# Kernel tuning notes

Hardware: AMD Instinct MI355X
Metric: run time of the kernel (lower is better)

The kernel has to match this reference:

```python
import jax, jax.numpy as jnp
import numpy as np

T, B, E, H = 2048, 2, 1024, 16

def setup_inputs() -> dict:
    rng = jax.random.key(0)
    ks = jax.random.split(rng, 7)
    s = 0.02
    return {
        "query": jax.random.normal(ks[0], (T, B, E), jnp.float32),
        "key": jax.random.normal(ks[1], (T, B, E), jnp.float32),
        "value": jax.random.normal(ks[2], (T, B, E), jnp.float32),
        "in_proj_weight": jax.random.normal(ks[3], (3 * E, E), jnp.float32) * s,
        "in_proj_bias": jax.random.normal(ks[4], (3 * E,), jnp.float32) * s,
        "out_proj_weight": jax.random.normal(ks[5], (E, E), jnp.float32) * s,
        "out_proj_bias": jax.random.normal(ks[6], (E,), jnp.float32) * s,
    }

def reference(query, key, value, in_proj_weight, in_proj_bias, out_proj_weight, out_proj_bias):
    tgt_len, bsz, embed_dim = query.shape
    num_heads = H
    head_dim = embed_dim // num_heads
    scaling = head_dim ** -0.5
    wq, wk, wv = jnp.split(in_proj_weight, 3, axis=0)
    bq, bk, bv = jnp.split(in_proj_bias, 3, axis=0)
    # projections: F.linear(x, W, b) = x @ W.T + b
    q = (query @ wq.T + bq) * scaling          # (T, B, E)
    k = key @ wk.T + bk                        # (S, B, E)
    v = value @ wv.T + bv                      # (S, B, E)
    # (len, B, E) -> (B*H, len, head_dim), matching torch view+transpose
    def to_heads(x):
        L = x.shape[0]
        return x.reshape(L, bsz * num_heads, head_dim).transpose(1, 0, 2)
    q, k, v = to_heads(q), to_heads(k), to_heads(v)
    scores = jnp.einsum('bqd,bkd->bqk', q, k)  # (B*H, T, S)
    attn = jax.nn.softmax(scores, axis=-1)
    out = jnp.einsum('bqk,bkd->bqd', attn, v)  # (B*H, T, head_dim)
    out = out.transpose(1, 0, 2).reshape(tgt_len, bsz, embed_dim)
    out = out @ out_proj_weight.T + out_proj_bias
    return out
```

## Files before the change

kernel.cpp:

```cpp
#include <hip/hip_runtime.h>
#include <cstdint>
#include <cstddef>

#define QSCALE 0.18033688011112042f

typedef __attribute__((ext_vector_type(8))) short bf16x8;
typedef __attribute__((ext_vector_type(4))) float f32x4;

#define MFMA(a, b, c) __builtin_amdgcn_mfma_f32_16x16x32_bf16(a, b, c, 0, 0, 0)

#define PIPE_SYNC() do {                                   \
    asm volatile("s_waitcnt vmcnt(0)" ::: "memory");       \
    __builtin_amdgcn_sched_barrier(0);                     \
    __builtin_amdgcn_s_barrier();                          \
    __builtin_amdgcn_sched_barrier(0);                     \
  } while (0)

typedef union { unsigned int u[4]; bf16x8 b; } pku;

__device__ __forceinline__ unsigned short cvt_bf16(float x) {
  union { float f; unsigned int u; } v;
  v.f = x;
  unsigned int r = v.u + 0x7FFFu + ((v.u >> 16) & 1u);
  return (unsigned short)(r >> 16);
}

__device__ __forceinline__ void gll16(const void* g, void* l) {
  __builtin_amdgcn_global_load_lds(
      (const __attribute__((address_space(1))) unsigned int*)g,
      (__attribute__((address_space(3))) unsigned int*)l, 16, 0, 0);
}

__device__ __forceinline__ float fast_exp2(float x) {
#if __has_builtin(__builtin_amdgcn_exp2f)
  return __builtin_amdgcn_exp2f(x);
#else
  float r; asm("v_exp_f32 %0, %1" : "=v"(r) : "v"(x)); return r;
#endif
}

__device__ __forceinline__ unsigned int pack_bf16(float lo, float hi) {
  union { float f; unsigned int u; } a, b;
  a.f = lo; b.f = hi;
  return __builtin_amdgcn_perm(b.u + 0x8000u, a.u + 0x8000u, 0x07060302u);
}

__global__ void cvt_all(const float* __restrict__ q,
                        const float* __restrict__ k,
                        const float* __restrict__ v,
                        const float* __restrict__ ipw,
                        const float* __restrict__ opw,
                        unsigned short* __restrict__ dst) {
  const size_t i = ((size_t)blockIdx.x * 256 + threadIdx.x) * 8;
  const float* src;
  float scale = 1.0f;
  if (i < 4194304) src = q + i;
  else if (i < 8388608) src = k + (i - 4194304);
  else if (i < 12582912) src = v + (i - 8388608);
  else {
    const size_t w = i - 12582912;
    if (w < 3145728) { src = ipw + w; if (w < 1048576) scale = QSCALE; }
    else src = opw + (w - 3145728);
  }
  float4 a = *(const float4*)src;
  float4 b = *(const float4*)(src + 4);
  uint4 o;
  o.x = cvt_bf16(a.x * scale) | ((unsigned int)cvt_bf16(a.y * scale) << 16);
  o.y = cvt_bf16(a.z * scale) | ((unsigned int)cvt_bf16(a.w * scale) << 16);
  o.z = cvt_bf16(b.x * scale) | ((unsigned int)cvt_bf16(b.y * scale) << 16);
  o.w = cvt_bf16(b.z * scale) | ((unsigned int)cvt_bf16(b.w * scale) << 16);
  *(uint4*)(dst + i) = o;
}

__global__ __launch_bounds__(256, 2) void gemm_qkv(
    const unsigned short* __restrict__ X,
    const unsigned short* __restrict__ W,
    const float* __restrict__ bias,
    unsigned short* __restrict__ Qh,
    unsigned short* __restrict__ Kh,
    unsigned short* __restrict__ Vt)
{
  __shared__ unsigned short S[2][16384];
  const int tid = threadIdx.x;
  const int wave = tid >> 6, lane = tid & 63;
  const int quad = lane >> 4, l16 = lane & 15;
  const int flat = blockIdx.x + (blockIdx.y << 3) + (blockIdx.z << 8);
  const int nf = (flat & 7) * 96 + (flat >> 3);
  const int z = nf >> 8;
  const int m0 = ((nf >> 3) & 31) * 128;
  const int n0 = (nf & 7) * 128;
  const unsigned short* Ab = X + (size_t)z * 4194304 + (size_t)m0 * 1024;
  const unsigned short* Bb = W + ((size_t)z * 1024 + n0) * 1024;
  const int wr = (wave >> 1) * 64, wc = (wave & 1) * 64;

  const f32x4 z4 = {0.f, 0.f, 0.f, 0.f};
  f32x4 acc[4][4];
#pragma unroll
  for (int i = 0; i < 4; ++i)
#pragma unroll
    for (int j = 0; j < 4; ++j) acc[i][j] = z4;

  auto stage = [&](int k0, int buf) {
#pragma unroll
    for (int j = 0; j < 4; ++j) {
      const int c = j * 256 + tid;
      const int row = c >> 3, pc = c & 7;
      const int kc = pc ^ (row & 7);
      gll16(Ab + (size_t)row * 1024 + k0 + kc * 8, &S[buf][c * 8]);
      gll16(Bb + (size_t)row * 1024 + k0 + kc * 8, &S[buf][8192 + c * 8]);
    }
  };

  stage(0, 0);

#pragma unroll 1
  for (int t = 0; t < 16; ++t) {
    const int cur = t & 1;
    PIPE_SYNC();
    if (t < 15) stage((t + 1) * 64, cur ^ 1);
    const unsigned short* As = S[cur];
    const unsigned short* Bs = S[cur] + 8192;
#pragma unroll
    for (int kk = 0; kk < 2; ++kk) {
      bf16x8 af[4], bfr[4];
#pragma unroll
      for (int rt = 0; rt < 4; ++rt) {
        const int row = wr + rt * 16 + l16;
        af[rt] = *(const bf16x8*)&As[row * 64 + ((kk * 4 + quad) ^ (row & 7)) * 8];
      }
#pragma unroll
      for (int ct = 0; ct < 4; ++ct) {
        const int row = wc + ct * 16 + l16;
        bfr[ct] = *(const bf16x8*)&Bs[row * 64 + ((kk * 4 + quad) ^ (row & 7)) * 8];
      }
#pragma unroll
      for (int rt = 0; rt < 4; ++rt)
#pragma unroll
        for (int ct = 0; ct < 4; ++ct)
          acc[rt][ct] = MFMA(af[rt], bfr[ct], acc[rt][ct]);
    }
  }

#pragma unroll
  for (int rt = 0; rt < 4; ++rt)
#pragma unroll
    for (int ct = 0; ct < 4; ++ct) {
      const int gn = n0 + wc + ct * 16 + l16;
      float bv = bias[z * 1024 + gn];
      if (z == 0) bv *= QSCALE;
      const int h = gn >> 6, d = gn & 63;
#pragma unroll
      for (int r = 0; r < 4; ++r) {
        const int gm = m0 + wr + rt * 16 + quad * 4 + r;
        const int t = gm >> 1, b = gm & 1;
        const int bh = b * 16 + h;
        const unsigned short o = cvt_bf16(acc[rt][ct][r] + bv);
        if (z == 0)      Qh[((size_t)bh * 2048 + t) * 64 + d] = o;
        else if (z == 1) Kh[((size_t)bh * 2048 + t) * 64 + d] = o;
        else {
          const int w32 = t & 31;
          const int tp = (t & ~31) | (((w32 >> 2) & 3) << 3) | ((w32 >> 4) << 2) | (w32 & 3);
          Vt[((size_t)bh * 64 + d) * 2048 + tp] = o;
        }
      }
    }
}

__global__ __launch_bounds__(256, 2) void attn(
    const unsigned short* __restrict__ Qh,
    const unsigned short* __restrict__ Kh,
    const unsigned short* __restrict__ Vt,
    unsigned short* __restrict__ O)
{
  __shared__ unsigned short KV[2][16384];
  __shared__ float Ls[128];
  const int tid = threadIdx.x;
  const int wave = tid >> 6, lane = tid & 63;
  const int quad = lane >> 4, l16 = lane & 15;
  const int pair = wave >> 1, kh = wave & 1;
  const int flat = blockIdx.x + (blockIdx.y << 4);
  const int nf = (flat & 7) * 64 + (flat >> 3);
  const int qt = nf & 15, bh = nf >> 4;
  const unsigned short* Qb = Qh + ((size_t)bh * 2048 + qt * 128 + pair * 64) * 64;
  const unsigned short* Kb = Kh + (size_t)bh * 2048 * 64;
  const unsigned short* Vb = Vt + (size_t)bh * 64 * 2048;

  bf16x8 qf[4][2];
#pragma unroll
  for (int g = 0; g < 4; ++g)
#pragma unroll
    for (int kk = 0; kk < 2; ++kk)
      qf[g][kk] = *(const bf16x8*)(Qb + (size_t)(g * 16 + l16) * 64 + kk * 32 + quad * 8);

  const unsigned short* kp[4];
  const unsigned short* vp[4];
  int klo[4], vlo[4];
#pragma unroll
  for (int j = 0; j < 4; ++j) {
    const int c = wave * 256 + j * 64 + lane;
    const int r = c >> 3, cc = c & 7;
    kp[j] = Kb + (size_t)r * 64 + (cc ^ (r & 7)) * 8;
    klo[j] = c * 8;
    const int r2 = c >> 4, cc2 = c & 15;
    vp[j] = Vb + (size_t)r2 * 2048 + (cc2 ^ (r2 & 15)) * 8;
    vlo[j] = 8192 + c * 8;
  }

  pku ones;
  ones.u[0] = ones.u[1] = ones.u[2] = ones.u[3] = 0x3F803F80u;

  const f32x4 z4 = {0.f, 0.f, 0.f, 0.f};
  f32x4 oacc[4][4];
  f32x4 lacc[4] = {z4, z4, z4, z4};
#pragma unroll
  for (int g = 0; g < 4; ++g)
#pragma unroll
    for (int c = 0; c < 4; ++c) oacc[g][c] = z4;

#pragma unroll
  for (int j = 0; j < 4; ++j) {
    gll16(kp[j], &KV[0][klo[j]]);
    gll16(vp[j], &KV[0][vlo[j]]);
    kp[j] += 128 * 64;
    vp[j] += 128;
  }

#pragma unroll 1
  for (int it = 0; it < 16; ++it) {
    const int cur = it & 1;
    PIPE_SYNC();
    if (it < 15) {
#pragma unroll
      for (int j = 0; j < 4; ++j) {
        gll16(kp[j], &KV[cur ^ 1][klo[j]]);
        gll16(vp[j], &KV[cur ^ 1][vlo[j]]);
        kp[j] += 128 * 64;
        vp[j] += 128;
      }
    }
    const unsigned short* Ks = KV[cur];
    const unsigned short* Vs = KV[cur] + 8192;

#pragma unroll
    for (int jj = 0; jj < 2; ++jj) {
      unsigned int pk0[4][2], pk1[4][2];
#pragma unroll
      for (int half = 0; half < 2; ++half) {
        const int ct = jj * 2 + half;
        const int R = kh * 64 + ct * 16 + l16;
        bf16x8 kfr[2];
#pragma unroll
        for (int kk = 0; kk < 2; ++kk)
          kfr[kk] = *(const bf16x8*)&Ks[R * 64 + ((kk * 4 + quad) ^ (R & 7)) * 8];
#pragma unroll
        for (int g = 0; g < 4; ++g) {
          f32x4 sv = z4;
          sv = MFMA(kfr[0], qf[g][0], sv);
          sv = MFMA(kfr[1], qf[g][1], sv);
          f32x4 p;
#pragma unroll
          for (int r = 0; r < 4; ++r) p[r] = fast_exp2(sv[r]);
          pk0[g][half] = pack_bf16(p[0], p[1]);
          pk1[g][half] = pack_bf16(p[2], p[3]);
        }
      }
      const int jjg = kh * 2 + jj;
#pragma unroll
      for (int ctd = 0; ctd < 4; ++ctd) {
        const int R = ctd * 16 + l16;
        const int phys = (jjg * 4 + quad) ^ (R & 15);
        const bf16x8 vv = *(const bf16x8*)&Vs[R * 128 + phys * 8];
#pragma unroll
        for (int g = 0; g < 4; ++g) {
          pku a;
          a.u[0] = pk0[g][0]; a.u[1] = pk1[g][0];
          a.u[2] = pk0[g][1]; a.u[3] = pk1[g][1];
          oacc[g][ctd] = MFMA(a.b, vv, oacc[g][ctd]);
        }
      }
#pragma unroll
      for (int g = 0; g < 4; ++g) {
        pku a;
        a.u[0] = pk0[g][0]; a.u[1] = pk1[g][0];
        a.u[2] = pk0[g][1]; a.u[3] = pk1[g][1];
        lacc[g] = MFMA(a.b, ones.b, lacc[g]);
      }
    }
  }

  __syncthreads();
  float* Fp = (float*)KV;
  if (kh == 1) {
#pragma unroll
    for (int g = 0; g < 4; ++g) {
#pragma unroll
      for (int ctd = 0; ctd < 4; ++ctd)
#pragma unroll
        for (int r = 0; r < 4; ++r)
          Fp[pair * 4096 + (g * 16 + quad * 4 + r) * 64 + ctd * 16 + l16] = oacc[g][ctd][r];
#pragma unroll
      for (int r = 0; r < 4; ++r)
        Ls[pair * 64 + g * 16 + quad * 4 + r] = lacc[g][r];
    }
  }
  __syncthreads();
  if (kh == 0) {
    const int b = bh >> 4, h = bh & 15;
#pragma unroll
    for (int g = 0; g < 4; ++g)
#pragma unroll
      for (int r = 0; r < 4; ++r) {
        const int ql = g * 16 + quad * 4 + r;
        const float lv = lacc[g][r] + Ls[pair * 64 + ql];
        const float inv = 1.0f / lv;
        const int t = qt * 128 + pair * 64 + ql;
#pragma unroll
        for (int ctd = 0; ctd < 4; ++ctd) {
          const float val = oacc[g][ctd][r] + Fp[pair * 4096 + ql * 64 + ctd * 16 + l16];
          O[((size_t)t * 2 + b) * 1024 + h * 64 + ctd * 16 + l16] = cvt_bf16(val * inv);
        }
      }
  }
}

__global__ __launch_bounds__(256, 2) void gemm_out(
    const unsigned short* __restrict__ A,
    const unsigned short* __restrict__ W,
    const float* __restrict__ bias,
    float* __restrict__ out)
{
  __shared__ unsigned short As[2][128 * 64];
  __shared__ unsigned short Bs[2][64 * 64];
  const int tid = threadIdx.x;
  const int wave = tid >> 6, lane = tid & 63;
  const int quad = lane >> 4, l16 = lane & 15;
  const int flat = blockIdx.x + (blockIdx.y << 4);
  const int nf = (flat & 7) * 64 + (flat >> 3);
  const int m0 = (nf >> 4) * 128;
  const int n0 = (nf & 15) * 64;
  const unsigned short* Ab = A + (size_t)m0 * 1024;
  const unsigned short* Bb = W + (size_t)n0 * 1024;
  const int wr = (wave >> 1) * 64, wc = (wave & 1) * 32;

  auto stage = [&](int k0, int buf) {
#pragma unroll
    for (int j = 0; j < 4; ++j) {
      const int c = j * 256 + tid;
      const int row = c >> 3, pc = c & 7;
      const int kc = pc ^ (row & 7);
      gll16(Ab + (size_t)row * 1024 + k0 + kc * 8, &As[buf][c * 8]);
    }
#pragma unroll
    for (int j = 0; j < 2; ++j) {
      const int c = j * 256 + tid;
      const int row = c >> 3, pc = c & 7;
      const int kc = pc ^ (row & 7);
      gll16(Bb + (size_t)row * 1024 + k0 + kc * 8, &Bs[buf][c * 8]);
    }
  };

  const f32x4 z4 = {0.f, 0.f, 0.f, 0.f};
  f32x4 acc[4][2];
#pragma unroll
  for (int i = 0; i < 4; ++i)
#pragma unroll
    for (int j = 0; j < 2; ++j) acc[i][j] = z4;

  stage(0, 0);

#pragma unroll 1
  for (int k0 = 0; k0 < 1024; k0 += 64) {
    const int cur = (k0 >> 6) & 1;
    PIPE_SYNC();
    if (k0 < 960) stage(k0 + 64, cur ^ 1);
#pragma unroll
    for (int kk = 0; kk < 2; ++kk) {
      bf16x8 af[4], bfr[2];
#pragma unroll
      for (int rt = 0; rt < 4; ++rt) {
        const int row = wr + rt * 16 + l16;
        af[rt] = *(const bf16x8*)&As[cur][row * 64 + ((kk * 4 + quad) ^ (row & 7)) * 8];
      }
#pragma unroll
      for (int ct = 0; ct < 2; ++ct) {
        const int row = wc + ct * 16 + l16;
        bfr[ct] = *(const bf16x8*)&Bs[cur][row * 64 + ((kk * 4 + quad) ^ (row & 7)) * 8];
      }
#pragma unroll
      for (int rt = 0; rt < 4; ++rt)
#pragma unroll
        for (int ct = 0; ct < 2; ++ct)
          acc[rt][ct] = MFMA(af[rt], bfr[ct], acc[rt][ct]);
    }
  }

#pragma unroll
  for (int rt = 0; rt < 4; ++rt)
#pragma unroll
    for (int ct = 0; ct < 2; ++ct) {
      const int gn = n0 + wc + ct * 16 + l16;
      const float bv = bias[gn];
#pragma unroll
      for (int r = 0; r < 4; ++r) {
        const int gm = m0 + wr + rt * 16 + quad * 4 + r;
        out[(size_t)gm * 1024 + gn] = acc[rt][ct][r] + bv;
      }
    }
}

extern "C" void kernel_launch(void* const* d_in, const int* in_sizes, int n_in,
                              void* d_out, int out_size, void* d_ws, size_t ws_size,
                              hipStream_t stream) {
  const float* q   = (const float*)d_in[0];
  const float* k   = (const float*)d_in[1];
  const float* v   = (const float*)d_in[2];
  const float* ipw = (const float*)d_in[3];
  const float* ipb = (const float*)d_in[4];
  const float* opw = (const float*)d_in[5];
  const float* opb = (const float*)d_in[6];

  unsigned short* ws = (unsigned short*)d_ws;
  unsigned short* X  = ws;
  unsigned short* Wb = ws + 12582912;
  unsigned short* Wo = ws + 15728640;
  unsigned short* Qh = ws + 16777216;
  unsigned short* Kh = ws + 20971520;
  unsigned short* Vx = ws + 25165824;
  unsigned short* Oa = ws + 29360128;

  cvt_all<<<dim3(8192), 256, 0, stream>>>(q, k, v, ipw, opw, ws);
  gemm_qkv<<<dim3(8, 32, 3), 256, 0, stream>>>(X, Wb, ipb, Qh, Kh, Vx);
  attn<<<dim3(16, 32), 256, 0, stream>>>(Qh, Kh, Vx, Oa);
  gemm_out<<<dim3(16, 32), 256, 0, stream>>>(Oa, Wo, opb, (float*)d_out);
}
```

Measured before the change: 211.4 us.

## Enlarge QKV GEMM tiles to 256x256 with 8 waves and phased staging

The QKV projection GEMM moves from 128x128 tiles with 4 waves to 256x256 tiles with 8 waves (512 threads) and 128 KB of LDS double buffering. The next K slice is loaded in four quarter-stages interleaved with four compute phases separated by lightweight barriers. This is meant to raise arithmetic intensity per loaded byte and overlap loads with MFMA work. It also adds s_setprio around MFMA regions in the GEMM and in the attention PV loop. The costs are fewer blocks (192), heavier register pressure, and a risk of LDS-limited occupancy of one block per CU.

After: 224.4 us. 1.06x slower.

```diff
diff --git a/kernel.cpp b/kernel.cpp
--- a/kernel.cpp
+++ b/kernel.cpp
@@ -11,6 +11,12 @@
 
 #define PIPE_SYNC() do {                                   \
     asm volatile("s_waitcnt vmcnt(0)" ::: "memory");       \
+    __builtin_amdgcn_sched_barrier(0);                     \
+    __builtin_amdgcn_s_barrier();                          \
+    __builtin_amdgcn_sched_barrier(0);                     \
+  } while (0)
+
+#define PHASE_SYNC() do {                                  \
     __builtin_amdgcn_sched_barrier(0);                     \
     __builtin_amdgcn_s_barrier();                          \
     __builtin_amdgcn_sched_barrier(0);                     \
@@ -72,7 +78,7 @@
   *(uint4*)(dst + i) = o;
 }
 
-__global__ __launch_bounds__(256, 2) void gemm_qkv(
+__global__ __launch_bounds__(512, 2) void gemm_qkv(
     const unsigned short* __restrict__ X,
     const unsigned short* __restrict__ W,
     const float* __restrict__ bias,
@@ -80,81 +86,94 @@
     unsigned short* __restrict__ Kh,
     unsigned short* __restrict__ Vt)
 {
-  __shared__ unsigned short S[2][16384];
+  __shared__ unsigned short S[2][32768];
   const int tid = threadIdx.x;
   const int wave = tid >> 6, lane = tid & 63;
   const int quad = lane >> 4, l16 = lane & 15;
-  const int flat = blockIdx.x + (blockIdx.y << 3) + (blockIdx.z << 8);
-  const int nf = (flat & 7) * 96 + (flat >> 3);
-  const int z = nf >> 8;
-  const int m0 = ((nf >> 3) & 31) * 128;
-  const int n0 = (nf & 7) * 128;
+  const int mr = wave >> 2, nc = wave & 3;
+  const int flat = blockIdx.x + (blockIdx.y << 3);
+  const int nf = (flat & 7) * 24 + (flat >> 3);
+  const int z = nf >> 6;
+  const int rem = nf & 63;
+  const int m0 = (rem >> 2) << 8;
+  const int n0 = (rem & 3) << 8;
   const unsigned short* Ab = X + (size_t)z * 4194304 + (size_t)m0 * 1024;
   const unsigned short* Bb = W + ((size_t)z * 1024 + n0) * 1024;
-  const int wr = (wave >> 1) * 64, wc = (wave & 1) * 64;
 
   const f32x4 z4 = {0.f, 0.f, 0.f, 0.f};
-  f32x4 acc[4][4];
-#pragma unroll
-  for (int i = 0; i < 4; ++i)
+  f32x4 acc[8][4];
+#pragma unroll
+  for (int i = 0; i < 8; ++i)
 #pragma unroll
     for (int j = 0; j < 4; ++j) acc[i][j] = z4;
 
-  auto stage = [&](int k0, int buf) {
-#pragma unroll
-    for (int j = 0; j < 4; ++j) {
-      const int c = j * 256 + tid;
-      const int row = c >> 3, pc = c & 7;
+  auto stage_half = [&](int s, int k0, int buf) {
+    const unsigned short* srcb = (s < 2) ? Ab : Bb;
+    const int rowoff = (s & 1) * 128;
+    const int ldsoff = (s < 2) ? 0 : 16384;
+#pragma unroll
+    for (int j = 0; j < 2; ++j) {
+      const int c = j * 512 + tid;
+      const int r128 = c >> 3, pc = c & 7;
+      const int row = rowoff + r128;
       const int kc = pc ^ (row & 7);
-      gll16(Ab + (size_t)row * 1024 + k0 + kc * 8, &S[buf][c * 8]);
-      gll16(Bb + (size_t)row * 1024 + k0 + kc * 8, &S[buf][8192 + c * 8]);
+      gll16(srcb + (size_t)row * 1024 + k0 + kc * 8,
+            &S[buf][ldsoff + rowoff * 64 + c * 8]);
     }
   };
 
-  stage(0, 0);
+#pragma unroll
+  for (int s = 0; s < 4; ++s) stage_half(s, 0, 0);
+  PIPE_SYNC();
 
 #pragma unroll 1
   for (int t = 0; t < 16; ++t) {
     const int cur = t & 1;
-    PIPE_SYNC();
-    if (t < 15) stage((t + 1) * 64, cur ^ 1);
-    const unsigned short* As = S[cur];
-    const unsigned short* Bs = S[cur] + 8192;
-#pragma unroll
-    for (int kk = 0; kk < 2; ++kk) {
-      bf16x8 af[4], bfr[4];
-#pragma unroll
-      for (int rt = 0; rt < 4; ++rt) {
-        const int row = wr + rt * 16 + l16;
-        af[rt] = *(const bf16x8*)&As[row * 64 + ((kk * 4 + quad) ^ (row & 7)) * 8];
-      }
-#pragma unroll
-      for (int ct = 0; ct < 4; ++ct) {
-        const int row = wc + ct * 16 + l16;
-        bfr[ct] = *(const bf16x8*)&Bs[row * 64 + ((kk * 4 + quad) ^ (row & 7)) * 8];
-      }
-#pragma unroll
-      for (int rt = 0; rt < 4; ++rt)
-#pragma unroll
-        for (int ct = 0; ct < 4; ++ct)
-          acc[rt][ct] = MFMA(af[rt], bfr[ct], acc[rt][ct]);
-    }
-  }
-
-#pragma unroll
-  for (int rt = 0; rt < 4; ++rt)
-#pragma unroll
-    for (int ct = 0; ct < 4; ++ct) {
-      const int gn = n0 + wc + ct * 16 + l16;
+#pragma unroll
+    for (int p = 0; p < 4; ++p) {
+      if (t < 15) stage_half(p, (t + 1) * 64, cur ^ 1);
+      const int qr = p >> 1, qc = p & 1;
+      __builtin_amdgcn_s_setprio(1);
+#pragma unroll
+      for (int kk = 0; kk < 2; ++kk) {
+        bf16x8 af[4], bfr[2];
+#pragma unroll
+        for (int rt = 0; rt < 4; ++rt) {
+          const int Ar = mr * 128 + qr * 64 + rt * 16 + l16;
+          af[rt] = *(const bf16x8*)&S[cur][Ar * 64 + ((kk * 4 + quad) ^ (Ar & 7)) * 8];
+        }
+#pragma unroll
+        for (int ct = 0; ct < 2; ++ct) {
+          const int Br = nc * 64 + qc * 32 + ct * 16 + l16;
+          bfr[ct] = *(const bf16x8*)&S[cur][16384 + Br * 64 + ((kk * 4 + quad) ^ (Br & 7)) * 8];
+        }
+#pragma unroll
+        for (int rt = 0; rt < 4; ++rt)
+#pragma unroll
+          for (int ct = 0; ct < 2; ++ct)
+            acc[qr * 4 + rt][qc * 2 + ct] = MFMA(af[rt], bfr[ct], acc[qr * 4 + rt][qc * 2 + ct]);
+      }
+      __builtin_amdgcn_s_setprio(0);
+      if (p == 3) { PIPE_SYNC(); } else { PHASE_SYNC(); }
+    }
+  }
+
+#pragma unroll
+  for (int ar = 0; ar < 8; ++ar)
+#pragma unroll
+    for (int ac = 0; ac < 4; ++ac) {
+      const int col = nc * 64 + (ac >> 1) * 32 + (ac & 1) * 16 + l16;
+      const int gn = n0 + col;
       float bv = bias[z * 1024 + gn];
       if (z == 0) bv *= QSCALE;
       const int h = gn >> 6, d = gn & 63;
+      const int rowb = mr * 128 + (ar >> 2) * 64 + (ar & 3) * 16 + quad * 4;
 #pragma unroll
       for (int r = 0; r < 4; ++r) {
-        const int gm = m0 + wr + rt * 16 + quad * 4 + r;
+        const int gm = m0 + rowb + r;
         const int t = gm >> 1, b = gm & 1;
         const int bh = b * 16 + h;
-        const unsigned short o = cvt_bf16(acc[rt][ct][r] + bv);
+        const unsigned short o = cvt_bf16(acc[ar][ac][r] + bv);
         if (z == 0)      Qh[((size_t)bh * 2048 + t) * 64 + d] = o;
         else if (z == 1) Kh[((size_t)bh * 2048 + t) * 64 + d] = o;
         else {
@@ -265,6 +284,7 @@
         }
       }
       const int jjg = kh * 2 + jj;
+      __builtin_amdgcn_s_setprio(1);
 #pragma unroll
       for (int ctd = 0; ctd < 4; ++ctd) {
         const int R = ctd * 16 + l16;
@@ -285,6 +305,7 @@
         a.u[2] = pk0[g][1]; a.u[3] = pk1[g][1];
         lacc[g] = MFMA(a.b, ones.b, lacc[g]);
       }
+      __builtin_amdgcn_s_setprio(0);
     }
   }
 
@@ -429,7 +450,7 @@
   unsigned short* Oa = ws + 29360128;
 
   cvt_all<<<dim3(8192), 256, 0, stream>>>(q, k, v, ipw, opw, ws);
-  gemm_qkv<<<dim3(8, 32, 3), 256, 0, stream>>>(X, Wb, ipb, Qh, Kh, Vx);
+  gemm_qkv<<<dim3(8, 24), 512, 0, stream>>>(X, Wb, ipb, Qh, Kh, Vx);
   attn<<<dim3(16, 32), 256, 0, stream>>>(Qh, Kh, Vx, Oa);
   gemm_out<<<dim3(16, 32), 256, 0, stream>>>(Oa, Wo, opb, (float*)d_out);
 }
```
